# Kernel tuning notes

Hardware: AMD Instinct MI355X
Metric: run time of the kernel (lower is better)

## Reference

```python
import jax, jax.numpy as jnp
import numpy as np

C = 64  # channels fixed by module

def conv1x1(x, W, b):
    # x: [B,C,H,W], W: [C_out,C_in], b: [C_out]
    return jnp.einsum('bchw,oc->bohw', x, W) + b[None, :, None, None]

def setup_inputs() -> dict:
    key = jax.random.key(0)
    ks = jax.random.split(key, 16)
    B, H, W = 4, 64, 64
    inp = {
        'x_latter': jax.random.normal(ks[0], (B, C, H, W), jnp.float32),
        'x': jax.random.normal(ks[1], (B, C, H, W), jnp.float32),
    }
    scale = 1.0 / np.sqrt(C)
    names = ['high', 'low', 'value', 'e_conv', 'mid', 'latter']
    for i, n in enumerate(names):
        inp[f'W_{n}'] = jax.random.normal(ks[2 + 2 * i], (C, C), jnp.float32) * scale
        inp[f'b_{n}'] = jax.random.normal(ks[3 + 2 * i], (C,), jnp.float32) * 0.01
    return inp

def reference(x_latter, x, W_high, b_high, W_low, b_low, W_value, b_value,
              W_e_conv, b_e_conv, W_mid, b_mid, W_latter, b_latter):
    b, c, h, w = x_latter.shape
    hw = h * w
    # stage 1: channel-normalized spatial attention
    xl_hi = conv1x1(x_latter, W_high, b_high).reshape(b, c, hw)          # [b,c,hw]
    x_low = conv1x1(x, W_low, b_low).reshape(b, c, hw).transpose(0, 2, 1)  # [b,hw,c]
    p = jnp.einsum('bnc,bcm->bnm', x_low, xl_hi)                          # [b,hw,hw]
    p = jax.nn.softmax(p, axis=1)  # torch Softmax(dim=1) over first hw axis
    v = conv1x1(x, W_value, b_value).reshape(b, c, hw).transpose(0, 2, 1)  # [b,hw,c]
    e = jnp.einsum('bnm,bmc->bnc', p, v) + x_low                          # [b,hw,c]
    e = e.transpose(0, 2, 1).reshape(b, c, h, w)                          # [b,c,h,w]
    e = conv1x1(e, W_e_conv, b_e_conv).reshape(b, c, hw)                  # [b,c,hw]
    # stage 2: channel-channel attention
    xl2 = conv1x1(x_latter, W_latter, b_latter).reshape(b, c, hw).transpose(0, 2, 1)  # [b,hw,c]
    t = jnp.einsum('bcn,bnd->bcd', e, xl2)                                # [b,c,c]
    t = jax.nn.softmax(t, axis=1)
    x_mid = conv1x1(x, W_mid, b_mid).reshape(b, c, hw).transpose(0, 2, 1)  # [b,hw,c]
    out = jnp.einsum('bnc,bcd->bnd', x_mid, t)                            # [b,hw,c]
    return out.transpose(0, 2, 1).reshape(b, c, h, w)
```

## Files before the change

kernel.cpp:

```cpp
#include <hip/hip_runtime.h>
#include <math.h>

#define BATCH 4
#define CH 64
#define HW 4096

typedef __attribute__((ext_vector_type(8))) short short8;
typedef __attribute__((ext_vector_type(4))) float f32x4;
typedef __attribute__((ext_vector_type(4))) float float4v;

#define MFMA(a, b, c) __builtin_amdgcn_mfma_f32_16x16x32_bf16(a, b, c, 0, 0, 0)

__device__ __forceinline__ short f2bf(float f) {
    unsigned u = __builtin_bit_cast(unsigned, f);
    u += 0x7fffu + ((u >> 16) & 1u);
    return (short)(u >> 16);
}
__device__ __forceinline__ float bf2f(short s) {
    unsigned u = ((unsigned)(unsigned short)s) << 16;
    return __builtin_bit_cast(float, u);
}
__device__ __forceinline__ void gld16(const short* g, short* l) {
    __builtin_amdgcn_global_load_lds(
        (const __attribute__((address_space(1))) unsigned int*)g,
        (__attribute__((address_space(3))) unsigned int*)l, 16, 0, 0);
}

__global__ __launch_bounds__(256) void splitX(
    const float* __restrict__ x, const float* __restrict__ xl,
    short* __restrict__ XFh, short* __restrict__ XFl)
{
    int src = blockIdx.z, b = blockIdx.y, bx = blockIdx.x;
    const float* X = src ? xl : x;
    int t = threadIdx.x, wv = t >> 6, ln = t & 63;
    int nt = bx * 4 + wv;
    int n = (nt << 4) + (ln & 15);
    int g = ln >> 4;
    size_t sb = ((size_t)(src * BATCH + b) * 256 + nt) * 2;
    #pragma unroll
    for (int kt = 0; kt < 2; kt++) {
        short8 h, l;
        #pragma unroll
        for (int j = 0; j < 8; j++) {
            float v = X[(size_t)(b * 64 + kt * 32 + g * 8 + j) * HW + n];
            short hh = f2bf(v);
            h[j] = hh;
            l[j] = f2bf(v - bf2f(hh));
        }
        *(short8*)(XFh + (sb + kt) * 512 + (size_t)ln * 8) = h;
        *(short8*)(XFl + (sb + kt) * 512 + (size_t)ln * 8) = l;
    }
}

__global__ __launch_bounds__(256) void convm(
    const short* __restrict__ XFh, const short* __restrict__ XFl,
    const float* __restrict__ Wlow, const float* __restrict__ blow,
    const float* __restrict__ Wval, const float* __restrict__ bval,
    const float* __restrict__ Wmid, const float* __restrict__ bmid,
    const float* __restrict__ Wlat, const float* __restrict__ blat,
    const float* __restrict__ Whigh, const float* __restrict__ bhigh,
    float* __restrict__ XLOW, float* __restrict__ XMID, float* __restrict__ XL2,
    short* __restrict__ PAh, short* __restrict__ PAl,
    short* __restrict__ PBh, short* __restrict__ PBl,
    short* __restrict__ PVh, short* __restrict__ PVl)
{
    int mode = blockIdx.z, b = blockIdx.y, bx = blockIdx.x;
    const float* W; const float* bias; int src;
    switch (mode) {
        case 0:  W = Wlow;  bias = blow;  src = 0; break;
        case 1:  W = Wval;  bias = bval;  src = 0; break;
        case 2:  W = Wmid;  bias = bmid;  src = 0; break;
        case 3:  W = Wlat;  bias = blat;  src = 1; break;
        default: W = Whigh; bias = bhigh; src = 1; break;
    }
    int t = threadIdx.x, wv = t >> 6, ln = t & 63;
    int row = ln & 15, g = ln >> 4;

    short8 Wh[4][2], Wlo[4][2];
    #pragma unroll
    for (int ot = 0; ot < 4; ot++)
        #pragma unroll
        for (int kt = 0; kt < 2; kt++) {
            const float* wp = W + (ot * 16 + row) * 64 + kt * 32 + g * 8;
            short8 h, l;
            #pragma unroll
            for (int j = 0; j < 8; j++) {
                float v = wp[j];
                short hh = f2bf(v);
                h[j] = hh;
                l[j] = f2bf(v - bf2f(hh));
            }
            Wh[ot][kt] = h; Wlo[ot][kt] = l;
        }

    int nt = bx * 4 + wv;
    size_t xb = ((size_t)(src * BATCH + b) * 256 + nt) * 2;
    short8 Bh[2], Bl[2];
    #pragma unroll
    for (int kt = 0; kt < 2; kt++) {
        Bh[kt] = *(const short8*)(XFh + (xb + kt) * 512 + (size_t)ln * 8);
        Bl[kt] = *(const short8*)(XFl + (xb + kt) * 512 + (size_t)ln * 8);
    }

    f32x4 acc[4];
    #pragma unroll
    for (int ot = 0; ot < 4; ot++) {
        #pragma unroll
        for (int r = 0; r < 4; r++) acc[ot][r] = bias[ot * 16 + g * 4 + r];
    }
    #pragma unroll
    for (int ot = 0; ot < 4; ot++)
        #pragma unroll
        for (int kt = 0; kt < 2; kt++) {
            acc[ot] = MFMA(Wh[ot][kt], Bh[kt], acc[ot]);
            acc[ot] = MFMA(Wh[ot][kt], Bl[kt], acc[ot]);
            acc[ot] = MFMA(Wlo[ot][kt], Bh[kt], acc[ot]);
        }

    __shared__ float Ld[64][65];
    #pragma unroll
    for (int ot = 0; ot < 4; ot++)
        #pragma unroll
        for (int r = 0; r < 4; r++)
            Ld[wv * 16 + (ln & 15)][ot * 16 + g * 4 + r] = acc[ot][r];
    __syncthreads();

    int n0 = bx * 64;
    if (mode == 0 || mode == 2 || mode == 3) {
        float* outp = (mode == 0) ? XLOW : (mode == 2) ? XMID : XL2;
        int n = t >> 2, o0 = (t & 3) * 16;
        float vout[16];
        #pragma unroll
        for (int k = 0; k < 16; k++) vout[k] = Ld[n][o0 + k];
        float* gp = outp + ((size_t)b * HW + n0 + n) * 64 + o0;
        #pragma unroll
        for (int k = 0; k < 4; k++)
            *(float4v*)(gp + k * 4) = *(float4v*)(vout + k * 4);
    }
    if (mode == 0 || mode == 4) {
        short* Ph = (mode == 0) ? PAh : PBh;
        short* Pl = (mode == 0) ? PAl : PBl;
        #pragma unroll
        for (int kt = 0; kt < 2; kt++) {
            short8 h, l;
            #pragma unroll
            for (int j = 0; j < 8; j++) {
                float v = Ld[wv * 16 + (ln & 15)][kt * 32 + g * 8 + j];
                short hh = f2bf(v);
                h[j] = hh;
                l[j] = f2bf(v - bf2f(hh));
            }
            size_t blob = (((size_t)b * 256 + bx * 4 + wv) * 2 + kt) * 512 + (size_t)ln * 8;
            *(short8*)(Ph + blob) = h;
            *(short8*)(Pl + blob) = l;
        }
    }
    if (mode == 1) {
        int ktm_l = wv >> 1;
        int ct0 = (wv & 1) * 2;
        #pragma unroll
        for (int cc = 0; cc < 2; cc++) {
            int ct = ct0 + cc;
            int c = ct * 16 + (ln & 15);
            short8 h, l;
            #pragma unroll
            for (int j = 0; j < 8; j++) {
                float v = Ld[(ktm_l * 2 + (j >> 2)) * 16 + g * 4 + (j & 3)][c];
                short hh = f2bf(v);
                h[j] = hh;
                l[j] = f2bf(v - bf2f(hh));
            }
            size_t blob = (((size_t)b * 128 + bx * 2 + ktm_l) * 4 + ct) * 512 + (size_t)ln * 8;
            *(short8*)(PVh + blob) = h;
            *(short8*)(PVl + blob) = l;
        }
    }
}

__global__ __launch_bounds__(256) void zpass2(
    const short* __restrict__ PAh, const short* __restrict__ PAl,
    const short* __restrict__ PBh, const short* __restrict__ PBl,
    float* __restrict__ Zp)
{
    int bid = blockIdx.x;
    int sw = (bid & 7) * 128 + (bid >> 3);
    int mchunk = sw & 63, nc = (sw >> 6) & 3, b = sw >> 8;
    int t = threadIdx.x, wv = t >> 6, ln = t & 63;
    short8 bh[4][2], bl[4][2];
    #pragma unroll
    for (int msub = 0; msub < 4; msub++)
        #pragma unroll
        for (int kt = 0; kt < 2; kt++) {
            size_t o = ((size_t)(b * 256 + mchunk * 4 + msub) * 2 + kt) * 512 + ln * 8;
            bh[msub][kt] = *(const short8*)(PBh + o);
            bl[msub][kt] = *(const short8*)(PBl + o);
        }
    float zacc[4] = {0.f, 0.f, 0.f, 0.f};
    for (int s = 0; s < 16; s++) {
        int nt = nc * 64 + s * 4 + wv;
        size_t ab = ((size_t)(b * 256 + nt) * 2) * 512 + ln * 8;
        short8 ah0 = *(const short8*)(PAh + ab);
        short8 ah1 = *(const short8*)(PAh + ab + 512);
        short8 al0 = *(const short8*)(PAl + ab);
        short8 al1 = *(const short8*)(PAl + ab + 512);
        #pragma unroll
        for (int msub = 0; msub < 4; msub++) {
            f32x4 acc = {0.f, 0.f, 0.f, 0.f};
            acc = MFMA(ah0, bh[msub][0], acc);
            acc = MFMA(ah1, bh[msub][1], acc);
            acc = MFMA(ah0, bl[msub][0], acc);
            acc = MFMA(ah1, bl[msub][1], acc);
            acc = MFMA(al0, bh[msub][0], acc);
            acc = MFMA(al1, bh[msub][1], acc);
            zacc[msub] += __expf(acc[0]) + __expf(acc[1]) + __expf(acc[2]) + __expf(acc[3]);
        }
    }
    #pragma unroll
    for (int msub = 0; msub < 4; msub++) {
        zacc[msub] += __shfl_xor(zacc[msub], 16, 64);
        zacc[msub] += __shfl_xor(zacc[msub], 32, 64);
    }
    __shared__ float sZ[4][64];
    if (ln < 16) {
        #pragma unroll
        for (int msub = 0; msub < 4; msub++) sZ[wv][msub * 16 + ln] = zacc[msub];
    }
    __syncthreads();
    if (t < 64) {
        float z = sZ[0][t] + sZ[1][t] + sZ[2][t] + sZ[3][t];
        Zp[((size_t)(b * 4 + nc)) * 4096 + mchunk * 64 + t] = z;
    }
}

__global__ __launch_bounds__(256, 1) void epass6(
    const short* __restrict__ PAh, const short* __restrict__ PAl,
    const short* __restrict__ PBh, const short* __restrict__ PBl,
    const short* __restrict__ PVh, const short* __restrict__ PVl,
    const float* __restrict__ Zp, float* __restrict__ Ep)
{
    int bid = blockIdx.x;
    int sw = (bid & 7) * 32 + (bid >> 3);
    int b = sw >> 6, mseg = (sw >> 4) & 3, nb = sw & 15;
    int t = threadIdx.x, wv = t >> 6, ln = t & 63;
    int lnm = ln & 15, lnr = ln >> 4;

    __shared__ __align__(16) short sB[2][2][4096];
    __shared__ __align__(16) short sV[2][2][4096];
    __shared__ float sZi[1024];

    for (int k = t; k < 1024; k += 256) {
        int m = mseg * 1024 + k;
        float z = Zp[((size_t)(b * 4 + 0)) * 4096 + m]
                + Zp[((size_t)(b * 4 + 1)) * 4096 + m]
                + Zp[((size_t)(b * 4 + 2)) * 4096 + m]
                + Zp[((size_t)(b * 4 + 3)) * 4096 + m];
        sZi[k] = 1.f / z;
    }

    short8 Lh[4][2], Ll[4][2];
    #pragma unroll
    for (int rt = 0; rt < 4; rt++)
        #pragma unroll
        for (int kt = 0; kt < 2; kt++) {
            int nt = nb * 16 + wv * 4 + rt;
            size_t base = ((size_t)(b * 256 + nt) * 2 + kt) * 512 + ln * 8;
            Lh[rt][kt] = *(const short8*)(PAh + base);
            Ll[rt][kt] = *(const short8*)(PAl + base);
        }

    f32x4 acc_e[4][4];
    #pragma unroll
    for (int rt = 0; rt < 4; rt++)
        #pragma unroll
        for (int ct = 0; ct < 4; ct++) acc_e[rt][ct] = (f32x4){0.f, 0.f, 0.f, 0.f};

    const int mc0 = mseg * 16;
    #define STAGE(bufi, ii) { \
        size_t bb = (size_t)b * 262144 + (size_t)(mc0 + (ii)) * 4096; \
        gld16(PBh + bb + t * 8,        &sB[bufi][0][wv * 512]); \
        gld16(PBh + bb + 2048 + t * 8, &sB[bufi][0][2048 + wv * 512]); \
        gld16(PBl + bb + t * 8,        &sB[bufi][1][wv * 512]); \
        gld16(PBl + bb + 2048 + t * 8, &sB[bufi][1][2048 + wv * 512]); \
        gld16(PVh + bb + t * 8,        &sV[bufi][0][wv * 512]); \
        gld16(PVh + bb + 2048 + t * 8, &sV[bufi][0][2048 + wv * 512]); \
        gld16(PVl + bb + t * 8,        &sV[bufi][1][wv * 512]); \
        gld16(PVl + bb + 2048 + t * 8, &sV[bufi][1][2048 + wv * 512]); }

    STAGE(0, 0);
    __syncthreads();
    for (int i = 0; i < 16; i++) {
        int cur = i & 1;
        __builtin_amdgcn_s_barrier();
        if (i < 15) {
            STAGE(cur ^ 1, i + 1);
            asm volatile("s_waitcnt vmcnt(8)" ::: "memory");
        } else {
            asm volatile("s_waitcnt vmcnt(0)" ::: "memory");
        }
        __builtin_amdgcn_sched_barrier(0);

        #pragma unroll
        for (int ktm = 0; ktm < 2; ktm++) {
            f32x4 wf[4][2];
            #pragma unroll
            for (int ms = 0; ms < 2; ms++) {
                int msub = ktm * 2 + ms;
                const short8 bh0 = *(const short8*)&sB[cur][0][(msub * 2 + 0) * 512 + ln * 8];
                const short8 bh1 = *(const short8*)&sB[cur][0][(msub * 2 + 1) * 512 + ln * 8];
                const short8 bl0 = *(const short8*)&sB[cur][1][(msub * 2 + 0) * 512 + ln * 8];
                const short8 bl1 = *(const short8*)&sB[cur][1][(msub * 2 + 1) * 512 + ln * 8];
                const f32x4 vz = *(const f32x4*)&sZi[i * 64 + msub * 16 + lnr * 4];
                #pragma unroll
                for (int rt = 0; rt < 4; rt++) {
                    f32x4 acc = {0.f, 0.f, 0.f, 0.f};
                    acc = MFMA(bh0, Lh[rt][0], acc);
                    acc = MFMA(bh1, Lh[rt][1], acc);
                    acc = MFMA(bh0, Ll[rt][0], acc);
                    acc = MFMA(bh1, Ll[rt][1], acc);
                    acc = MFMA(bl0, Lh[rt][0], acc);
                    acc = MFMA(bl1, Lh[rt][1], acc);
                    #pragma unroll
                    for (int r = 0; r < 4; r++)
                        wf[rt][ms][r] = __expf(acc[r]) * vz[r];
                }
            }
            short8 pah[4], pal[4];
            #pragma unroll
            for (int rt = 0; rt < 4; rt++) {
                short8 h, l;
                #pragma unroll
                for (int j = 0; j < 8; j++) {
                    float w = wf[rt][j >> 2][j & 3];
                    short hh = f2bf(w);
                    h[j] = hh;
                    l[j] = f2bf(w - bf2f(hh));
                }
                pah[rt] = h; pal[rt] = l;
            }
            #pragma unroll
            for (int ct = 0; ct < 4; ct++) {
                const short8 vh = *(const short8*)&sV[cur][0][(ktm * 4 + ct) * 512 + ln * 8];
                const short8 vl = *(const short8*)&sV[cur][1][(ktm * 4 + ct) * 512 + ln * 8];
                #pragma unroll
                for (int rt = 0; rt < 4; rt++) {
                    acc_e[rt][ct] = MFMA(pah[rt], vh, acc_e[rt][ct]);
                    acc_e[rt][ct] = MFMA(pah[rt], vl, acc_e[rt][ct]);
                    acc_e[rt][ct] = MFMA(pal[rt], vh, acc_e[rt][ct]);
                }
            }
        }
    }
    #undef STAGE

    float* ep = Ep + ((size_t)mseg * BATCH + b) * HW * 64;
    #pragma unroll
    for (int rt = 0; rt < 4; rt++) {
        int n0 = (nb * 16 + wv * 4 + rt) * 16 + lnr * 4;
        #pragma unroll
        for (int ct = 0; ct < 4; ct++) {
            #pragma unroll
            for (int r = 0; r < 4; r++)
                ep[(size_t)(n0 + r) * 64 + ct * 16 + lnm] = acc_e[rt][ct][r];
        }
    }
}

__global__ __launch_bounds__(256) void econv5(
    const float* __restrict__ Ep, const float* __restrict__ XLOW,
    const float* __restrict__ W, const float* __restrict__ bias,
    float* __restrict__ E2)
{
    const size_t SEG = (size_t)BATCH * HW * 64;
    int b = blockIdx.y, n0 = blockIdx.x * 64, t = threadIdx.x;
    __shared__ float Wl[64][64];
    __shared__ float El[64][65];
    for (int i = t; i < 4096; i += 256) Wl[i >> 6][i & 63] = W[i];
    for (int i = t; i < 4096; i += 256) {
        int nl = i >> 6, c = i & 63;
        size_t idx = ((size_t)b * HW + n0 + nl) * 64 + c;
        El[nl][c] = XLOW[idx] + Ep[idx] + Ep[SEG + idx] + Ep[2 * SEG + idx] + Ep[3 * SEG + idx];
    }
    __syncthreads();
    int nl = t & 63, og = t >> 6;
    for (int k = 0; k < 16; k++) {
        int o = og * 16 + k;
        float a0 = bias[o], a1 = 0.f, a2 = 0.f, a3 = 0.f;
        #pragma unroll
        for (int c = 0; c < 64; c += 4) {
            a0 += Wl[o][c]     * El[nl][c];
            a1 += Wl[o][c + 1] * El[nl][c + 1];
            a2 += Wl[o][c + 2] * El[nl][c + 2];
            a3 += Wl[o][c + 3] * El[nl][c + 3];
        }
        E2[((size_t)b * 64 + o) * HW + n0 + nl] = (a0 + a1) + (a2 + a3);
    }
}

__global__ __launch_bounds__(1024) void tmat(
    const float* __restrict__ E2, const float* __restrict__ XL2, float* __restrict__ T)
{
    int b = blockIdx.y, c = blockIdx.x, t = threadIdx.x;
    int d = t & 63, nl = t >> 6;
    const float* e = E2 + ((size_t)b * 64 + c) * HW;
    const float* x2 = XL2 + (size_t)b * HW * 64;
    float a0 = 0.f, a1 = 0.f;
    #pragma unroll 4
    for (int k = 0; k < 256; k += 2) {
        int na = k * 16 + nl, nb2 = na + 16;
        a0 += e[na] * x2[(size_t)na * 64 + d];
        a1 += e[nb2] * x2[(size_t)nb2 * 64 + d];
    }
    __shared__ float red[16][64];
    red[nl][d] = a0 + a1;
    __syncthreads();
    if (t < 64) {
        float s = 0.f;
        #pragma unroll
        for (int j = 0; j < 16; j++) s += red[j][t];
        T[((size_t)b * 64 + c) * 64 + t] = s;
    }
}

__global__ __launch_bounds__(64) void softT(
    const float* __restrict__ T, float* __restrict__ Ts)
{
    int d = blockIdx.x, b = blockIdx.y, c = threadIdx.x;
    float v = T[((size_t)b * 64 + c) * 64 + d];
    float M = v;
    #pragma unroll
    for (int o = 32; o > 0; o >>= 1) M = fmaxf(M, __shfl_xor(M, o, 64));
    float ez = __expf(v - M);
    float Z = ez;
    #pragma unroll
    for (int o = 32; o > 0; o >>= 1) Z += __shfl_xor(Z, o, 64);
    Ts[((size_t)b * 64 + c) * 64 + d] = ez / Z;
}

__global__ __launch_bounds__(256) void outk(
    const float* __restrict__ XMID, const float* __restrict__ Ts, float* __restrict__ out)
{
    int b = blockIdx.y, n0 = blockIdx.x * 64, t = threadIdx.x;
    __shared__ float Xm[64][65];
    __shared__ float Tl[64][64];
    for (int i = t; i < 4096; i += 256) {
        int nl = i >> 6, c = i & 63;
        Xm[nl][c] = XMID[((size_t)b * HW + n0 + nl) * 64 + c];
    }
    for (int i = t; i < 4096; i += 256) Tl[i >> 6][i & 63] = Ts[(size_t)b * 4096 + i];
    __syncthreads();
    int nl = t & 63, dg = t >> 6;
    float accs[16];
    #pragma unroll
    for (int k = 0; k < 16; k++) accs[k] = 0.f;
    for (int c = 0; c < 64; c++) {
        float xv = Xm[nl][c];
        #pragma unroll
        for (int k = 0; k < 16; k++) accs[k] += xv * Tl[c][dg * 16 + k];
    }
    #pragma unroll
    for (int k = 0; k < 16; k++) {
        int d = dg * 16 + k;
        out[((size_t)b * 64 + d) * HW + n0 + nl] = accs[k];
    }
}

extern "C" void kernel_launch(void* const* d_in, const int* in_sizes, int n_in,
                              void* d_out, int out_size, void* d_ws, size_t ws_size,
                              hipStream_t stream)
{
    const float* x_latter = (const float*)d_in[0];
    const float* x        = (const float*)d_in[1];
    const float* W_high = (const float*)d_in[2];  const float* b_high = (const float*)d_in[3];
    const float* W_low  = (const float*)d_in[4];  const float* b_low  = (const float*)d_in[5];
    const float* W_val  = (const float*)d_in[6];  const float* b_val  = (const float*)d_in[7];
    const float* W_ec   = (const float*)d_in[8];  const float* b_ec   = (const float*)d_in[9];
    const float* W_mid  = (const float*)d_in[10]; const float* b_mid  = (const float*)d_in[11];
    const float* W_lat  = (const float*)d_in[12]; const float* b_lat  = (const float*)d_in[13];
    float* outp = (float*)d_out;

    const size_t MAT = (size_t)BATCH * CH * HW;
    float* ws = (float*)d_ws;
    size_t off = 0;
    float* XLOW = ws + off; off += MAT;
    float* XMID = ws + off; off += MAT;
    float* XL2  = ws + off; off += MAT;
    float* Ep   = ws + off; off += 4 * MAT;
    float* Zp   = ws + off; off += (size_t)BATCH * 4 * HW;
    float* T    = ws + off; off += (size_t)BATCH * 64 * 64;
    float* Ts   = ws + off; off += (size_t)BATCH * 64 * 64;
    short* sp = (short*)(ws + off);
    short* PAh = sp; sp += MAT;
    short* PAl = sp; sp += MAT;
    short* PBh = sp; sp += MAT;
    short* PBl = sp; sp += MAT;
    short* PVh = sp; sp += MAT;
    short* PVl = sp; sp += MAT;
    float* E2  = (float*)PAh;
    short* XFh = (short*)Ep;
    short* XFl = XFh + 2 * BATCH * 262144;

    splitX<<<dim3(64, BATCH, 2), 256, 0, stream>>>(x, x_latter, XFh, XFl);
    convm<<<dim3(64, BATCH, 5), 256, 0, stream>>>(
        XFh, XFl, W_low, b_low, W_val, b_val, W_mid, b_mid, W_lat, b_lat,
        W_high, b_high, XLOW, XMID, XL2, PAh, PAl, PBh, PBl, PVh, PVl);
    zpass2<<<dim3(1024), 256, 0, stream>>>(PAh, PAl, PBh, PBl, Zp);
    epass6<<<dim3(256), 256, 0, stream>>>(PAh, PAl, PBh, PBl, PVh, PVl, Zp, Ep);
    econv5<<<dim3(64, BATCH), 256, 0, stream>>>(Ep, XLOW, W_ec, b_ec, E2);
    tmat<<<dim3(64, BATCH), 1024, 0, stream>>>(E2, XL2, T);
    softT<<<dim3(64, BATCH), 64, 0, stream>>>(T, Ts);
    outk<<<dim3(64, BATCH), 256, 0, stream>>>(XMID, Ts, outp);
}
```

Before: 156.4 us.

## Split epass over more m-segments with two blocks per CU and wave priorities

The attention-value kernel now splits the m (key) dimension into a runtime-chosen number of segments, 8 when the workspace is large enough and 4 otherwise. This doubles the workgroup count, and launch bounds now allow two blocks per CU, to improve CU fill and latency hiding. The hand-written vmcnt waits are replaced by an end-of-iteration __syncthreads, and s_setprio brackets are added around the MFMA bursts. In exchange, econv must reduce more partial Ep buffers from a relocated, larger workspace region, and the register cap from two blocks per CU may cause spills.

```diff
diff --git a/kernel.cpp b/kernel.cpp
--- a/kernel.cpp
+++ b/kernel.cpp
@@ -232,24 +232,26 @@
     }
 }
 
-__global__ __launch_bounds__(256, 1) void epass6(
+__global__ __launch_bounds__(256, 2) void epass7(
     const short* __restrict__ PAh, const short* __restrict__ PAl,
     const short* __restrict__ PBh, const short* __restrict__ PBl,
     const short* __restrict__ PVh, const short* __restrict__ PVl,
-    const float* __restrict__ Zp, float* __restrict__ Ep)
-{
+    const float* __restrict__ Zp, float* __restrict__ Ep, int nseg)
+{
+    int nwg = 16 * nseg * 4, cpx = nwg >> 3;
     int bid = blockIdx.x;
-    int sw = (bid & 7) * 32 + (bid >> 3);
-    int b = sw >> 6, mseg = (sw >> 4) & 3, nb = sw & 15;
+    int sw = (bid & 7) * cpx + (bid >> 3);
+    int nb = sw & 15, mseg = (sw >> 4) % nseg, b = sw / (16 * nseg);
+    int iters = 64 / nseg;
     int t = threadIdx.x, wv = t >> 6, ln = t & 63;
     int lnm = ln & 15, lnr = ln >> 4;
 
     __shared__ __align__(16) short sB[2][2][4096];
     __shared__ __align__(16) short sV[2][2][4096];
-    __shared__ float sZi[1024];
-
-    for (int k = t; k < 1024; k += 256) {
-        int m = mseg * 1024 + k;
+    __shared__ __align__(16) float sZi[1024];
+
+    for (int k = t; k < iters * 64; k += 256) {
+        int m = mseg * iters * 64 + k;
         float z = Zp[((size_t)(b * 4 + 0)) * 4096 + m]
                 + Zp[((size_t)(b * 4 + 1)) * 4096 + m]
                 + Zp[((size_t)(b * 4 + 2)) * 4096 + m]
@@ -274,7 +276,7 @@
         #pragma unroll
         for (int ct = 0; ct < 4; ct++) acc_e[rt][ct] = (f32x4){0.f, 0.f, 0.f, 0.f};
 
-    const int mc0 = mseg * 16;
+    const int mc0 = mseg * iters;
     #define STAGE(bufi, ii) { \
         size_t bb = (size_t)b * 262144 + (size_t)(mc0 + (ii)) * 4096; \
         gld16(PBh + bb + t * 8,        &sB[bufi][0][wv * 512]); \
@@ -288,16 +290,10 @@
 
     STAGE(0, 0);
     __syncthreads();
-    for (int i = 0; i < 16; i++) {
+
+    for (int i = 0; i < iters; i++) {
         int cur = i & 1;
-        __builtin_amdgcn_s_barrier();
-        if (i < 15) {
-            STAGE(cur ^ 1, i + 1);
-            asm volatile("s_waitcnt vmcnt(8)" ::: "memory");
-        } else {
-            asm volatile("s_waitcnt vmcnt(0)" ::: "memory");
-        }
-        __builtin_amdgcn_sched_barrier(0);
+        if (i + 1 < iters) STAGE(cur ^ 1, i + 1);
 
         #pragma unroll
         for (int ktm = 0; ktm < 2; ktm++) {
@@ -310,6 +306,7 @@
                 const short8 bl0 = *(const short8*)&sB[cur][1][(msub * 2 + 0) * 512 + ln * 8];
                 const short8 bl1 = *(const short8*)&sB[cur][1][(msub * 2 + 1) * 512 + ln * 8];
                 const f32x4 vz = *(const f32x4*)&sZi[i * 64 + msub * 16 + lnr * 4];
+                __builtin_amdgcn_s_setprio(1);
                 #pragma unroll
                 for (int rt = 0; rt < 4; rt++) {
                     f32x4 acc = {0.f, 0.f, 0.f, 0.f};
@@ -323,6 +320,7 @@
                     for (int r = 0; r < 4; r++)
                         wf[rt][ms][r] = __expf(acc[r]) * vz[r];
                 }
+                __builtin_amdgcn_s_setprio(0);
             }
             short8 pah[4], pal[4];
             #pragma unroll
@@ -337,6 +335,7 @@
                 }
                 pah[rt] = h; pal[rt] = l;
             }
+            __builtin_amdgcn_s_setprio(1);
             #pragma unroll
             for (int ct = 0; ct < 4; ct++) {
                 const short8 vh = *(const short8*)&sV[cur][0][(ktm * 4 + ct) * 512 + ln * 8];
@@ -348,7 +347,9 @@
                     acc_e[rt][ct] = MFMA(pal[rt], vh, acc_e[rt][ct]);
                 }
             }
-        }
+            __builtin_amdgcn_s_setprio(0);
+        }
+        __syncthreads();
     }
     #undef STAGE
 
@@ -368,7 +369,7 @@
 __global__ __launch_bounds__(256) void econv5(
     const float* __restrict__ Ep, const float* __restrict__ XLOW,
     const float* __restrict__ W, const float* __restrict__ bias,
-    float* __restrict__ E2)
+    float* __restrict__ E2, int nseg)
 {
     const size_t SEG = (size_t)BATCH * HW * 64;
     int b = blockIdx.y, n0 = blockIdx.x * 64, t = threadIdx.x;
@@ -378,7 +379,9 @@
     for (int i = t; i < 4096; i += 256) {
         int nl = i >> 6, c = i & 63;
         size_t idx = ((size_t)b * HW + n0 + nl) * 64 + c;
-        El[nl][c] = XLOW[idx] + Ep[idx] + Ep[SEG + idx] + Ep[2 * SEG + idx] + Ep[3 * SEG + idx];
+        float s = XLOW[idx];
+        for (int sg = 0; sg < nseg; sg++) s += Ep[sg * SEG + idx];
+        El[nl][c] = s;
     }
     __syncthreads();
     int nl = t & 63, og = t >> 6;
@@ -479,12 +482,16 @@
     float* outp = (float*)d_out;
 
     const size_t MAT = (size_t)BATCH * CH * HW;
+
+    const size_t fixed_f = 3 * MAT + (size_t)BATCH * 4 * HW + 2 * (size_t)BATCH * 64 * 64;
+    const size_t need8 = (fixed_f + 8 * MAT) * 4 + 6 * MAT * 2;
+    int nseg = (ws_size >= need8) ? 8 : 4;
+
     float* ws = (float*)d_ws;
     size_t off = 0;
     float* XLOW = ws + off; off += MAT;
     float* XMID = ws + off; off += MAT;
     float* XL2  = ws + off; off += MAT;
-    float* Ep   = ws + off; off += 4 * MAT;
     float* Zp   = ws + off; off += (size_t)BATCH * 4 * HW;
     float* T    = ws + off; off += (size_t)BATCH * 64 * 64;
     float* Ts   = ws + off; off += (size_t)BATCH * 64 * 64;
@@ -495,6 +502,7 @@
     short* PBl = sp; sp += MAT;
     short* PVh = sp; sp += MAT;
     short* PVl = sp; sp += MAT;
+    float* Ep  = (float*)sp;
     float* E2  = (float*)PAh;
     short* XFh = (short*)Ep;
     short* XFl = XFh + 2 * BATCH * 262144;
@@ -504,8 +512,9 @@
         XFh, XFl, W_low, b_low, W_val, b_val, W_mid, b_mid, W_lat, b_lat,
         W_high, b_high, XLOW, XMID, XL2, PAh, PAl, PBh, PBl, PVh, PVl);
     zpass2<<<dim3(1024), 256, 0, stream>>>(PAh, PAl, PBh, PBl, Zp);
-    epass6<<<dim3(256), 256, 0, stream>>>(PAh, PAl, PBh, PBl, PVh, PVl, Zp, Ep);
-    econv5<<<dim3(64, BATCH), 256, 0, stream>>>(Ep, XLOW, W_ec, b_ec, E2);
+    epass7<<<dim3(16 * nseg * 4), 256, 0, stream>>>(
+        PAh, PAl, PBh, PBl, PVh, PVl, Zp, Ep, nseg);
+    econv5<<<dim3(64, BATCH), 256, 0, stream>>>(Ep, XLOW, W_ec, b_ec, E2, nseg);
     tmat<<<dim3(64, BATCH), 1024, 0, stream>>>(E2, XL2, T);
     softT<<<dim3(64, BATCH), 64, 0, stream>>>(T, Ts);
     outk<<<dim3(64, BATCH), 256, 0, stream>>>(XMID, Ts, outp);
```

After: 178.2 us. 1.14x slower.
